# Optimization experiments

Measured on AMD Instinct MI355X. Metric: run time of the kernel, lower is better.

The kernel has to match this reference:

```python
import jax, jax.numpy as jnp
import numpy as np

K = 10          # neighbors, hard-coded in MLP1.forward
NEG_SLOPE = 0.2 # LeakyReLU slope
EPS = 1e-5      # BatchNorm2d default eps


def setup_inputs() -> dict:
    key = jax.random.key(0)
    k1, k2, k3, k4 = jax.random.split(key, 4)
    B, C, N = 8, 6, 4096
    x = jax.random.normal(k1, (B, C, N), dtype=jnp.float32)
    W = jax.random.normal(k2, (64, 6), dtype=jnp.float32) * 0.2      # conv1x1 weight (O, I)
    gamma = jax.random.uniform(k3, (64,), jnp.float32, 0.5, 1.5)     # BN weight
    beta = jax.random.normal(k4, (64,), dtype=jnp.float32) * 0.1     # BN bias
    return {"x": x, "W": W, "gamma": gamma, "beta": beta}


def _knn_idx(x3, k):
    # pairwise_distance[b,i,j] = -||x_i - x_j||^2 (as in the torch knn)
    inner = jnp.einsum('bdn,bdm->bnm', x3, x3)          # x_i . x_j
    xx = jnp.sum(x3 * x3, axis=1)                       # (B, N)
    pd = 2.0 * inner - xx[:, :, None] - xx[:, None, :]  # (B, N, N)
    _, idx = jax.lax.top_k(pd, k)                       # k nearest (incl. self)
    return idx                                          # (B, N, k) int32


def reference(x, W, gamma, beta):
    # x: (B, 6, N)
    idx = _knn_idx(x[:, :3], K)                          # (B, N, k)
    # gather neighbor features: feat[b,c,n,j] = x[b,c,idx[b,n,j]]
    feat = jax.vmap(lambda xb, ib: xb[:, ib])(x, idx)    # (B, 6, N, k)
    # center xyz over the k neighbors and scale by 10
    xyz = feat[:, :3]
    xyz = (xyz - jnp.mean(xyz, axis=-1, keepdims=True)) * 10.0
    feat = jnp.concatenate([xyz, feat[:, 3:]], axis=1)   # (B, 6, N, k)
    # 1x1 conv (6 -> 64), no bias
    y = jnp.einsum('oc,bcnk->bonk', W, feat)             # (B, 64, N, k)
    # BatchNorm2d in train mode: batch stats over (B, N, k), biased variance
    mu = jnp.mean(y, axis=(0, 2, 3), keepdims=True)
    var = jnp.mean((y - mu) ** 2, axis=(0, 2, 3), keepdims=True)
    y = (y - mu) * jax.lax.rsqrt(var + EPS)
    y = y * gamma[None, :, None, None] + beta[None, :, None, None]
    # LeakyReLU(0.2)
    y = jnp.where(y >= 0, y, NEG_SLOPE * y)
    # max over neighbors k
    y = jnp.max(y, axis=-1)                              # (B, 64, N)
    # global max + mean pooling over N, concat along last axis
    x1 = jnp.max(y, axis=-1)                             # (B, 64)
    x2 = jnp.mean(y, axis=-1)                            # (B, 64)
    return jnp.concatenate([x1, x2], axis=-1)            # (B, 128)
```

## Files before the change

kernel.cpp:

```cpp
#include <hip/hip_runtime.h>
#include <float.h>

#define K_NN 10
#define BATCH 8
#define CIN 6
#define NPTS 4096
#define COUT 64
#define NSEG 8
#define SEGLEN (NPTS / NSEG)
#define CHUNK 16
#define NCHUNK (SEGLEN / CHUNK)
#define CAP 32
#define NEG_SLOPE 0.2f
#define BN_EPS 1e-5f

static constexpr size_t OFF_IDX = 0;
static constexpr size_t OFF_PTS = OFF_IDX + (size_t)BATCH * K_NN * NPTS * sizeof(int);
static constexpr size_t OFF_Q   = OFF_PTS + (size_t)BATCH * NPTS * sizeof(float4);
static constexpr size_t SZ_Q    = (size_t)NSEG * BATCH * NPTS * K_NN * sizeof(int);
static constexpr size_t OFF_ST  = OFF_Q + SZ_Q;
static constexpr size_t OFF_SS  = OFF_ST + 32 * sizeof(double);

__device__ __forceinline__ float wave_sum(float v) {
#pragma unroll
    for (int m = 32; m >= 1; m >>= 1) v += __shfl_xor(v, m, 64);
    return v;
}
__device__ __forceinline__ float wave_max(float v) {
#pragma unroll
    for (int m = 32; m >= 1; m >>= 1) v = fmaxf(v, __shfl_xor(v, m, 64));
    return v;
}

__device__ __forceinline__ float distp(float4 qp, float4 c) {
    return fmaf(2.0f, fmaf(qp.z, c.z, fmaf(qp.y, c.y, qp.x * c.x)), -c.w);
}

__global__ __launch_bounds__(256) void prep_pts(const float* __restrict__ x,
                                                float4* __restrict__ pts,
                                                double* __restrict__ stats) {
    if (blockIdx.x == 0 && threadIdx.x < 27) stats[threadIdx.x] = 0.0;
    int t = blockIdx.x * 256 + threadIdx.x;
    int b = t >> 12;
    int n = t & (NPTS - 1);
    const float* xb = x + (size_t)b * CIN * NPTS;
    float x0 = xb[n];
    float x1 = xb[NPTS + n];
    float x2 = xb[2 * NPTS + n];
    pts[t] = make_float4(x0, x1, x2, x0 * x0 + x1 * x1 + x2 * x2);
}

__global__ __launch_bounds__(256) void knn_part(const float4* __restrict__ pts,
                                                int* __restrict__ part) {
    __shared__ unsigned short ssm[CAP * 256];
    int b = blockIdx.y;
    int s = blockIdx.z;
    int n = blockIdx.x * 256 + threadIdx.x;
    const float4* p = pts + (size_t)b * NPTS;
    float4 qp = p[n];

    int m0 = s * SEGLEN;

    float vals[K_NN];
#pragma unroll
    for (int j = 0; j < K_NN; j++) vals[j] = -FLT_MAX;

    for (int ch = 0; ch < NCHUNK; ch++) {
        float cmax = -FLT_MAX;
#pragma unroll
        for (int u = 0; u < CHUNK; u++) {
            float4 c = p[m0 + ch * CHUNK + u];
            cmax = fmaxf(cmax, distp(qp, c));
        }
        float t = cmax;
#pragma unroll
        for (int j = 0; j < K_NN; j++) {
            float hi = fmaxf(vals[j], t);
            t = fminf(vals[j], t);
            vals[j] = hi;
        }
    }
    float thr = vals[K_NN - 1];

    int cnt = 0;
#pragma unroll 8
    for (int mm = 0; mm < SEGLEN; mm++) {
        float4 c = p[m0 + mm];
        float d = distp(qp, c);
        int slot = min(cnt, CAP - 1);
        ssm[slot * 256 + threadIdx.x] = (unsigned short)(m0 + mm);
        cnt += (d >= thr) ? 1 : 0;
    }

    float fv[K_NN];
    int fi[K_NN];
#pragma unroll
    for (int j = 0; j < K_NN; j++) { fv[j] = -FLT_MAX; fi[j] = 0; }

    if (cnt <= CAP) {
        for (int j = 0; j < cnt; j++) {
            int m = ssm[j * 256 + threadIdx.x];
            float4 c = p[m];
            float d = distp(qp, c);
            if (d > fv[K_NN - 1]) {
                fv[K_NN - 1] = d;
                fi[K_NN - 1] = m;
#pragma unroll
                for (int t2 = K_NN - 1; t2 > 0; t2--) {
                    if (fv[t2] > fv[t2 - 1]) {
                        float tv = fv[t2]; fv[t2] = fv[t2 - 1]; fv[t2 - 1] = tv;
                        int ti = fi[t2]; fi[t2] = fi[t2 - 1]; fi[t2 - 1] = ti;
                    }
                }
            }
        }
    } else {
        for (int mm = 0; mm < SEGLEN; mm++) {
            int m = m0 + mm;
            float4 c = p[m];
            float d = distp(qp, c);
            if (d > fv[K_NN - 1]) {
                fv[K_NN - 1] = d;
                fi[K_NN - 1] = m;
#pragma unroll
                for (int t2 = K_NN - 1; t2 > 0; t2--) {
                    if (fv[t2] > fv[t2 - 1]) {
                        float tv = fv[t2]; fv[t2] = fv[t2 - 1]; fv[t2 - 1] = tv;
                        int ti = fi[t2]; fi[t2] = fi[t2 - 1]; fi[t2 - 1] = ti;
                    }
                }
            }
        }
    }

    int* o = part + (((size_t)s * BATCH + b) * K_NN) * NPTS + n;
#pragma unroll
    for (int j = 0; j < K_NN; j++) o[(size_t)j * NPTS] = fi[j];
}

__global__ __launch_bounds__(256) void merge_kernel(const float4* __restrict__ pts,
                                                    const int* __restrict__ part,
                                                    int* __restrict__ idxo) {
    int b = blockIdx.y;
    int n = blockIdx.x * 256 + threadIdx.x;
    const float4* p = pts + (size_t)b * NPTS;
    float4 qp = p[n];

    float vals[K_NN];
    int inds[K_NN];
#pragma unroll
    for (int j = 0; j < K_NN; j++) { vals[j] = -FLT_MAX; inds[j] = 0; }

#pragma unroll
    for (int s = 0; s < NSEG; s++) {
        const int* pp = part + (((size_t)s * BATCH + b) * K_NN) * NPTS + n;
#pragma unroll
        for (int j = 0; j < K_NN; j++) {
            int m = pp[(size_t)j * NPTS];
            float4 c = p[m];
            float d = distp(qp, c);
            if (d > vals[K_NN - 1]) {
                vals[K_NN - 1] = d;
                inds[K_NN - 1] = m;
#pragma unroll
                for (int t = K_NN - 1; t > 0; t--) {
                    if (vals[t] > vals[t - 1]) {
                        float tv = vals[t]; vals[t] = vals[t - 1]; vals[t - 1] = tv;
                        int ti = inds[t]; inds[t] = inds[t - 1]; inds[t - 1] = ti;
                    }
                }
            }
        }
    }

    int* o = idxo + (size_t)b * K_NN * NPTS + n;
#pragma unroll
    for (int j = 0; j < K_NN; j++) o[(size_t)j * NPTS] = inds[j];
}

__global__ __launch_bounds__(256) void feat_kernel(const float4* __restrict__ pts,
                                                   const float* __restrict__ x,
                                                   const float* __restrict__ W,
                                                   const int* __restrict__ idx,
                                                   float* __restrict__ q,
                                                   double* __restrict__ stats) {
    __shared__ float sW[COUT * CIN];
    __shared__ float sred[4][27];
    for (int i = threadIdx.x; i < COUT * CIN; i += 256) sW[i] = W[i];
    __syncthreads();

    int b = blockIdx.y;
    int n = blockIdx.x * 256 + threadIdx.x;
    const float* xb = x + (size_t)b * CIN * NPTS;
    const float4* p = pts + (size_t)b * NPTS;

    int nb[K_NN];
#pragma unroll
    for (int k = 0; k < K_NN; k++) nb[k] = idx[((size_t)b * K_NN + k) * NPTS + n];

    float f[CIN][K_NN];
#pragma unroll
    for (int k = 0; k < K_NN; k++) {
        float4 c = p[nb[k]];
        f[0][k] = c.x; f[1][k] = c.y; f[2][k] = c.z;
    }
#pragma unroll
    for (int c = 3; c < CIN; c++)
#pragma unroll
        for (int k = 0; k < K_NN; k++)
            f[c][k] = xb[c * NPTS + nb[k]];

#pragma unroll
    for (int c = 0; c < 3; c++) {
        float s = 0.f;
#pragma unroll
        for (int k = 0; k < K_NN; k++) s += f[c][k];
        float m = s / 10.0f;
#pragma unroll
        for (int k = 0; k < K_NN; k++) f[c][k] = (f[c][k] - m) * 10.0f;
    }

    float* qb = q + (size_t)b * COUT * NPTS + n;
#pragma unroll
    for (int o = 0; o < COUT; o++) {
        float w0 = sW[o * 6 + 0], w1 = sW[o * 6 + 1], w2 = sW[o * 6 + 2];
        float w3 = sW[o * 6 + 3], w4 = sW[o * 6 + 4], w5 = sW[o * 6 + 5];
        float mx = -FLT_MAX;
#pragma unroll
        for (int k = 0; k < K_NN; k++) {
            float y = w0 * f[0][k] + w1 * f[1][k] + w2 * f[2][k] +
                      w3 * f[3][k] + w4 * f[4][k] + w5 * f[5][k];
            mx = fmaxf(mx, y);
        }
        qb[(size_t)o * NPTS] = mx;
    }

    float s1[CIN];
#pragma unroll
    for (int c = 0; c < CIN; c++) {
        float s = 0.f;
#pragma unroll
        for (int k = 0; k < K_NN; k++) s += f[c][k];
        s1[c] = s;
    }
    float s2[21];
#pragma unroll
    for (int i = 0; i < 21; i++) s2[i] = 0.f;
#pragma unroll
    for (int k = 0; k < K_NN; k++) {
        int pp = 0;
#pragma unroll
        for (int c = 0; c < CIN; c++)
#pragma unroll
            for (int c2 = c; c2 < CIN; c2++) {
                s2[pp] += f[c][k] * f[c2][k];
                pp++;
            }
    }
#pragma unroll
    for (int c = 0; c < CIN; c++) s1[c] = wave_sum(s1[c]);
#pragma unroll
    for (int i = 0; i < 21; i++) s2[i] = wave_sum(s2[i]);

    int wv = threadIdx.x >> 6;
    int ln = threadIdx.x & 63;
    if (ln == 0) {
#pragma unroll
        for (int c = 0; c < CIN; c++) sred[wv][c] = s1[c];
#pragma unroll
        for (int i = 0; i < 21; i++) sred[wv][6 + i] = s2[i];
    }
    __syncthreads();
    if (threadIdx.x < 27) {
        float t = sred[0][threadIdx.x] + sred[1][threadIdx.x] +
                  sred[2][threadIdx.x] + sred[3][threadIdx.x];
        atomicAdd(&stats[threadIdx.x], (double)t);
    }
}

__global__ void stats_kernel(const double* __restrict__ stats,
                             const float* __restrict__ W,
                             const float* __restrict__ gamma,
                             const float* __restrict__ beta,
                             float* __restrict__ ss) {
    int o = threadIdx.x;
    const double minv = 1.0 / (double)((size_t)BATCH * NPTS * K_NN);
    double w[CIN];
#pragma unroll
    for (int c = 0; c < CIN; c++) w[c] = (double)W[o * CIN + c];
    double mu = 0.0;
#pragma unroll
    for (int c = 0; c < CIN; c++) mu += w[c] * stats[c];
    mu *= minv;
    double ey2 = 0.0;
    int p = 6;
#pragma unroll
    for (int c = 0; c < CIN; c++)
#pragma unroll
        for (int c2 = c; c2 < CIN; c2++) {
            double v = w[c] * w[c2] * stats[p];
            ey2 += (c2 == c) ? v : 2.0 * v;
            p++;
        }
    ey2 *= minv;
    double var = ey2 - mu * mu;
    float scale = gamma[o] * rsqrtf((float)var + BN_EPS);
    float shift = beta[o] - (float)mu * scale;
    ss[o] = scale;
    ss[COUT + o] = shift;
}

__global__ __launch_bounds__(256) void reduce_kernel(const float* __restrict__ q,
                                                     const float* __restrict__ ss,
                                                     float* __restrict__ out) {
    int o = blockIdx.x;
    int b = blockIdx.y;
    const float* qp = q + ((size_t)b * COUT + o) * NPTS;
    float scale = ss[o], shift = ss[COUT + o];
    float mx = -FLT_MAX, sm = 0.f;
    for (int i = threadIdx.x; i < NPTS; i += 256) {
        float z = scale * qp[i] + shift;
        z = (z >= 0.f) ? z : NEG_SLOPE * z;
        mx = fmaxf(mx, z);
        sm += z;
    }
    mx = wave_max(mx);
    sm = wave_sum(sm);
    __shared__ float smx[4], ssm2[4];
    int wv = threadIdx.x >> 6;
    int ln = threadIdx.x & 63;
    if (ln == 0) { smx[wv] = mx; ssm2[wv] = sm; }
    __syncthreads();
    if (threadIdx.x == 0) {
        float m = fmaxf(fmaxf(smx[0], smx[1]), fmaxf(smx[2], smx[3]));
        float s = ssm2[0] + ssm2[1] + ssm2[2] + ssm2[3];
        out[b * 2 * COUT + o] = m;
        out[b * 2 * COUT + COUT + o] = s * (1.0f / (float)NPTS);
    }
}

extern "C" void kernel_launch(void* const* d_in, const int* in_sizes, int n_in,
                              void* d_out, int out_size, void* d_ws, size_t ws_size,
                              hipStream_t stream) {
    const float* x     = (const float*)d_in[0];
    const float* W     = (const float*)d_in[1];
    const float* gamma = (const float*)d_in[2];
    const float* beta  = (const float*)d_in[3];
    float* out = (float*)d_out;

    char* ws = (char*)d_ws;
    int*    idx   = (int*)(ws + OFF_IDX);
    float4* pts   = (float4*)(ws + OFF_PTS);
    int*    part  = (int*)(ws + OFF_Q);
    float*  q     = (float*)(ws + OFF_Q);
    double* stats = (double*)(ws + OFF_ST);
    float*  ss    = (float*)(ws + OFF_SS);

    prep_pts<<<BATCH * NPTS / 256, 256, 0, stream>>>(x, pts, stats);
    knn_part<<<dim3(NPTS / 256, BATCH, NSEG), 256, 0, stream>>>(pts, part);
    merge_kernel<<<dim3(NPTS / 256, BATCH), 256, 0, stream>>>(pts, part, idx);
    feat_kernel<<<dim3(NPTS / 256, BATCH), 256, 0, stream>>>(pts, x, W, idx, q, stats);
    stats_kernel<<<1, COUT, 0, stream>>>(stats, W, gamma, beta, ss);
    reduce_kernel<<<dim3(COUT, BATCH), 256, 0, stream>>>(q, ss, out);
}
```

Baseline: 197.2 us.

## Replace KNN candidate shared-memory buffer with bitmask scan and shrink block sizes

The second KNN pass now builds a 32-bit mask of candidates above the threshold per 32-point word and walks its set bits with clz, instead of staging candidate indices in a capped shared-memory buffer with a full-rescan fallback. Points are pre-scaled by 2 so the distance becomes three FMAs. The chunk max uses a tree of max3 ops. Merge and feat kernels use smaller blocks (64 and 128 threads) to spread work over more CUs. The bitmask pass recomputes candidate distances and adds divergent while loops.

```diff
diff --git a/kernel.cpp b/kernel.cpp
--- a/kernel.cpp
+++ b/kernel.cpp
@@ -10,7 +10,7 @@
 #define SEGLEN (NPTS / NSEG)
 #define CHUNK 16
 #define NCHUNK (SEGLEN / CHUNK)
-#define CAP 32
+#define NWORD (SEGLEN / 32)
 #define NEG_SLOPE 0.2f
 #define BN_EPS 1e-5f
 
@@ -32,8 +32,12 @@
     return v;
 }
 
-__device__ __forceinline__ float distp(float4 qp, float4 c) {
-    return fmaf(2.0f, fmaf(qp.z, c.z, fmaf(qp.y, c.y, qp.x * c.x)), -c.w);
+__device__ __forceinline__ float distp(float qx, float qy, float qz, float4 c) {
+    return fmaf(c.x, qx, fmaf(c.y, qy, fmaf(c.z, qz, -c.w)));
+}
+
+__device__ __forceinline__ float fmax3(float a, float b, float c) {
+    return fmaxf(fmaxf(a, b), c);
 }
 
 __global__ __launch_bounds__(256) void prep_pts(const float* __restrict__ x,
@@ -47,17 +51,17 @@
     float x0 = xb[n];
     float x1 = xb[NPTS + n];
     float x2 = xb[2 * NPTS + n];
-    pts[t] = make_float4(x0, x1, x2, x0 * x0 + x1 * x1 + x2 * x2);
+    pts[t] = make_float4(2.0f * x0, 2.0f * x1, 2.0f * x2, x0 * x0 + x1 * x1 + x2 * x2);
 }
 
 __global__ __launch_bounds__(256) void knn_part(const float4* __restrict__ pts,
                                                 int* __restrict__ part) {
-    __shared__ unsigned short ssm[CAP * 256];
     int b = blockIdx.y;
     int s = blockIdx.z;
     int n = blockIdx.x * 256 + threadIdx.x;
     const float4* p = pts + (size_t)b * NPTS;
-    float4 qp = p[n];
+    float4 q4 = p[n];
+    float qx = 0.5f * q4.x, qy = 0.5f * q4.y, qz = 0.5f * q4.z;
 
     int m0 = s * SEGLEN;
 
@@ -66,13 +70,16 @@
     for (int j = 0; j < K_NN; j++) vals[j] = -FLT_MAX;
 
     for (int ch = 0; ch < NCHUNK; ch++) {
-        float cmax = -FLT_MAX;
-#pragma unroll
-        for (int u = 0; u < CHUNK; u++) {
-            float4 c = p[m0 + ch * CHUNK + u];
-            cmax = fmaxf(cmax, distp(qp, c));
-        }
-        float t = cmax;
+        const float4* cp = p + (m0 + ch * CHUNK);
+        float d[CHUNK];
+#pragma unroll
+        for (int u = 0; u < CHUNK; u++) d[u] = distp(qx, qy, qz, cp[u]);
+        float a0 = fmax3(d[0], d[1], d[2]);
+        float a1 = fmax3(d[3], d[4], d[5]);
+        float a2 = fmax3(d[6], d[7], d[8]);
+        float a3 = fmax3(d[9], d[10], d[11]);
+        float a4 = fmax3(d[12], d[13], d[14]);
+        float t = fmaxf(fmax3(fmax3(a0, a1, a2), a3, a4), d[15]);
 #pragma unroll
         for (int j = 0; j < K_NN; j++) {
             float hi = fmaxf(vals[j], t);
@@ -82,26 +89,26 @@
     }
     float thr = vals[K_NN - 1];
 
-    int cnt = 0;
-#pragma unroll 8
-    for (int mm = 0; mm < SEGLEN; mm++) {
-        float4 c = p[m0 + mm];
-        float d = distp(qp, c);
-        int slot = min(cnt, CAP - 1);
-        ssm[slot * 256 + threadIdx.x] = (unsigned short)(m0 + mm);
-        cnt += (d >= thr) ? 1 : 0;
-    }
-
     float fv[K_NN];
     int fi[K_NN];
 #pragma unroll
     for (int j = 0; j < K_NN; j++) { fv[j] = -FLT_MAX; fi[j] = 0; }
 
-    if (cnt <= CAP) {
-        for (int j = 0; j < cnt; j++) {
-            int m = ssm[j * 256 + threadIdx.x];
+    for (int w = 0; w < NWORD; w++) {
+        const float4* cp = p + (m0 + w * 32);
+        unsigned int mask = 0u;
+#pragma unroll
+        for (int u = 0; u < 32; u++) {
+            float d = distp(qx, qy, qz, cp[u]);
+            mask = (mask << 1) | (d >= thr ? 1u : 0u);
+        }
+        int base = m0 + w * 32;
+        while (mask) {
+            int j = __builtin_clz(mask);
+            mask ^= (0x80000000u >> j);
+            int m = base + j;
             float4 c = p[m];
-            float d = distp(qp, c);
+            float d = distp(qx, qy, qz, c);
             if (d > fv[K_NN - 1]) {
                 fv[K_NN - 1] = d;
                 fi[K_NN - 1] = m;
@@ -114,23 +121,6 @@
                 }
             }
         }
-    } else {
-        for (int mm = 0; mm < SEGLEN; mm++) {
-            int m = m0 + mm;
-            float4 c = p[m];
-            float d = distp(qp, c);
-            if (d > fv[K_NN - 1]) {
-                fv[K_NN - 1] = d;
-                fi[K_NN - 1] = m;
-#pragma unroll
-                for (int t2 = K_NN - 1; t2 > 0; t2--) {
-                    if (fv[t2] > fv[t2 - 1]) {
-                        float tv = fv[t2]; fv[t2] = fv[t2 - 1]; fv[t2 - 1] = tv;
-                        int ti = fi[t2]; fi[t2] = fi[t2 - 1]; fi[t2 - 1] = ti;
-                    }
-                }
-            }
-        }
     }
 
     int* o = part + (((size_t)s * BATCH + b) * K_NN) * NPTS + n;
@@ -138,13 +128,14 @@
     for (int j = 0; j < K_NN; j++) o[(size_t)j * NPTS] = fi[j];
 }
 
-__global__ __launch_bounds__(256) void merge_kernel(const float4* __restrict__ pts,
-                                                    const int* __restrict__ part,
-                                                    int* __restrict__ idxo) {
+__global__ __launch_bounds__(64) void merge_kernel(const float4* __restrict__ pts,
+                                                   const int* __restrict__ part,
+                                                   int* __restrict__ idxo) {
     int b = blockIdx.y;
-    int n = blockIdx.x * 256 + threadIdx.x;
+    int n = blockIdx.x * 64 + threadIdx.x;
     const float4* p = pts + (size_t)b * NPTS;
-    float4 qp = p[n];
+    float4 q4 = p[n];
+    float qx = 0.5f * q4.x, qy = 0.5f * q4.y, qz = 0.5f * q4.z;
 
     float vals[K_NN];
     int inds[K_NN];
@@ -158,7 +149,7 @@
         for (int j = 0; j < K_NN; j++) {
             int m = pp[(size_t)j * NPTS];
             float4 c = p[m];
-            float d = distp(qp, c);
+            float d = distp(qx, qy, qz, c);
             if (d > vals[K_NN - 1]) {
                 vals[K_NN - 1] = d;
                 inds[K_NN - 1] = m;
@@ -178,19 +169,19 @@
     for (int j = 0; j < K_NN; j++) o[(size_t)j * NPTS] = inds[j];
 }
 
-__global__ __launch_bounds__(256) void feat_kernel(const float4* __restrict__ pts,
+__global__ __launch_bounds__(128) void feat_kernel(const float4* __restrict__ pts,
                                                    const float* __restrict__ x,
                                                    const float* __restrict__ W,
                                                    const int* __restrict__ idx,
                                                    float* __restrict__ q,
                                                    double* __restrict__ stats) {
     __shared__ float sW[COUT * CIN];
-    __shared__ float sred[4][27];
-    for (int i = threadIdx.x; i < COUT * CIN; i += 256) sW[i] = W[i];
+    __shared__ float sred[2][27];
+    for (int i = threadIdx.x; i < COUT * CIN; i += 128) sW[i] = W[i];
     __syncthreads();
 
     int b = blockIdx.y;
-    int n = blockIdx.x * 256 + threadIdx.x;
+    int n = blockIdx.x * 128 + threadIdx.x;
     const float* xb = x + (size_t)b * CIN * NPTS;
     const float4* p = pts + (size_t)b * NPTS;
 
@@ -202,7 +193,7 @@
 #pragma unroll
     for (int k = 0; k < K_NN; k++) {
         float4 c = p[nb[k]];
-        f[0][k] = c.x; f[1][k] = c.y; f[2][k] = c.z;
+        f[0][k] = 0.5f * c.x; f[1][k] = 0.5f * c.y; f[2][k] = 0.5f * c.z;
     }
 #pragma unroll
     for (int c = 3; c < CIN; c++)
@@ -272,8 +263,7 @@
     }
     __syncthreads();
     if (threadIdx.x < 27) {
-        float t = sred[0][threadIdx.x] + sred[1][threadIdx.x] +
-                  sred[2][threadIdx.x] + sred[3][threadIdx.x];
+        float t = sred[0][threadIdx.x] + sred[1][threadIdx.x];
         atomicAdd(&stats[threadIdx.x], (double)t);
     }
 }
@@ -358,8 +348,8 @@
 
     prep_pts<<<BATCH * NPTS / 256, 256, 0, stream>>>(x, pts, stats);
     knn_part<<<dim3(NPTS / 256, BATCH, NSEG), 256, 0, stream>>>(pts, part);
-    merge_kernel<<<dim3(NPTS / 256, BATCH), 256, 0, stream>>>(pts, part, idx);
-    feat_kernel<<<dim3(NPTS / 256, BATCH), 256, 0, stream>>>(pts, x, W, idx, q, stats);
+    merge_kernel<<<dim3(NPTS / 64, BATCH), 64, 0, stream>>>(pts, part, idx);
+    feat_kernel<<<dim3(NPTS / 128, BATCH), 128, 0, stream>>>(pts, x, W, idx, q, stats);
     stats_kernel<<<1, COUT, 0, stream>>>(stats, W, gamma, beta, ss);
     reduce_kernel<<<dim3(COUT, BATCH), 256, 0, stream>>>(q, ss, out);
 }
```

Measured after the change: 198.1 us. About the same (+0.4%).
